# Optimization experiments

Hardware: AMD Instinct MI355X
Metric: run time of the kernel (lower is better)

Reference implementation:

```python
import jax, jax.numpy as jnp
import numpy as np

EPS = 1e-5


def _whiten(feature):
    # ZCA whitening per sample (WCT): f_w = U diag(s^-1/2) U^T (f - mean)
    b, c, h, w = feature.shape
    f = feature.reshape(b, c, h * w)
    mean = f.mean(axis=-1, keepdims=True)
    f = f - mean
    cov = jnp.einsum('bcx,bdx->bcd', f, f) / (h * w - 1)
    s, u = jnp.linalg.eigh(cov)
    s = jnp.maximum(s, EPS)
    out = jnp.einsum('bcd,bd,bed,bex->bcx', u, s ** -0.5, u, f)
    return out.reshape(b, c, h, w)


def _color(feature, target):
    # ZCA coloring: f_c = Ut diag(st^1/2) Ut^T (f - mean_f) + mean_t
    b, c, h, w = feature.shape
    f = feature.reshape(b, c, h * w)
    f = f - f.mean(axis=-1, keepdims=True)
    t = target.reshape(b, c, -1)
    tmean = t.mean(axis=-1, keepdims=True)
    tc = t - tmean
    cov = jnp.einsum('bcx,bdx->bcd', tc, tc) / (tc.shape[-1] - 1)
    s, u = jnp.linalg.eigh(cov)
    s = jnp.maximum(s, EPS)
    out = jnp.einsum('bcd,bd,bed,bex->bcx', u, s ** 0.5, u, f) + tmean
    return out.reshape(b, c, h, w)


def _patches(f, p):
    # [b,c,h,w] -> [b,c,h,w,p*p], same ordering as torch unfold(2,p).unfold(3,p)
    pad = (p - 1) // 2
    b, c, h, w = f.shape
    fp = jnp.pad(f, ((0, 0), (0, 0), (pad, pad), (pad, pad)))
    return jnp.stack([fp[:, :, i:i + h, j:j + w] for i in range(p) for j in range(p)], axis=-1)


def reference(content_feature, style_feature, style_strength, patch_size):
    p = int(patch_size)
    pad = (p - 1) // 2
    nc = _whiten(content_feature)
    ns = _whiten(style_feature)
    b, c, h, w = nc.shape
    n = h * w  # one style kernel per style spatial location (stride 1)

    # style kernels [b, n, c, p, p] and their L2 norms over (c,p,p)
    sk = _patches(ns, p).transpose(0, 2, 3, 1, 4).reshape(b, n, c, p, p)
    knorm = jnp.sqrt(jnp.sum(sk ** 2, axis=(2, 3, 4), keepdims=True))
    skn = (sk / knorm).reshape(b, n, c, p * p)

    # patch matching score == conv2d of content with normalized style kernels
    cp = _patches(nc, p)                              # [b,c,h,w,p*p]
    score = jnp.einsum('bchwk,bnck->bnhw', cp, skn)   # [b,n,h,w]

    # argmax one-hot -> gather the best-matching (un-normalized) style patch
    idx = jnp.argmax(score, axis=1)                   # [b,h,w]
    sel = jax.vmap(lambda k, i: k[i])(sk, idx.reshape(b, -1))  # [b,hw,c,p,p]
    sel = sel.reshape(b, h, w, c, p, p).transpose(0, 3, 1, 2, 4, 5)  # [b,c,h,w,p,p]

    # overlap-add == conv_transpose2d(one_hot, kernels, padding=p-1) on padded input
    buf = jnp.zeros((b, c, h + p - 1, w + p - 1), dtype=sel.dtype)
    for di in range(p):
        for dj in range(p):
            buf = buf.at[:, :, di:di + h, dj:dj + w].add(sel[:, :, :, :, di, dj])
    recon = buf[:, :, pad:pad + h, pad:pad + w]

    # overlap counts (norm_deconvolution)
    m = jnp.zeros((h + p - 1, w + p - 1), dtype=sel.dtype)
    for di in range(p):
        for dj in range(p):
            m = m.at[di:di + h, dj:dj + w].add(1.0)
    norm = m[pad:pad + h, pad:pad + w]

    reassembled = recon / norm[None, None]
    stylized = _color(reassembled, style_feature)
    return (1.0 - style_strength) * content_feature + style_strength * stylized


def setup_inputs():
    key = jax.random.key(0)
    k1, k2 = jax.random.split(key)
    B, C, H, W = 2, 256, 48, 48
    return {
        'content_feature': jax.random.normal(k1, (B, C, H, W), jnp.float32),
        'style_feature': jax.random.normal(k2, (B, C, H, W), jnp.float32),
        'style_strength': jnp.float32(1.0),
        'patch_size': 3,
    }
```

## Files before the change

kernel.cpp:

```cpp
#include <hip/hip_runtime.h>

constexpr int B_  = 2;
constexpr int C_  = 256;
constexpr int H_  = 48;
constexpr int W_  = 48;
constexpr int N_  = H_ * W_;
constexpr int PH_ = H_ + 2;
constexpr int PW_ = W_ + 2;
constexpr int NP_ = PH_ * PW_;
constexpr int CC_ = C_ * C_;
constexpr int NCH_ = 36;
constexpr int NC_  = N_ / NCH_;
constexpr int NSIT_ = 6;
constexpr int KCH_ = 9;

__device__ inline float waveRed(float v) {
  #pragma unroll
  for (int o = 32; o > 0; o >>= 1) v += __shfl_down(v, o);
  return v;
}

#define GEMM64_COMPUTE(sAT, sB, acc, ty, tx)                        \
  _Pragma("unroll")                                                 \
  for (int kk = 0; kk < 16; kk++) {                                 \
    float4 a = *(const float4*)&sAT[kk][(ty) * 4];                  \
    float4 b = *(const float4*)&sB[kk][(tx) * 4];                   \
    acc[0][0] += a.x * b.x; acc[0][1] += a.x * b.y;                 \
    acc[0][2] += a.x * b.z; acc[0][3] += a.x * b.w;                 \
    acc[1][0] += a.y * b.x; acc[1][1] += a.y * b.y;                 \
    acc[1][2] += a.y * b.z; acc[1][3] += a.y * b.w;                 \
    acc[2][0] += a.z * b.x; acc[2][1] += a.z * b.y;                 \
    acc[2][2] += a.z * b.z; acc[2][3] += a.z * b.w;                 \
    acc[3][0] += a.w * b.x; acc[3][1] += a.w * b.y;                 \
    acc[3][2] += a.w * b.z; acc[3][3] += a.w * b.w;                 \
  }


__global__ __launch_bounds__(256) void center_kernel(
    const float* __restrict__ content, const float* __restrict__ style,
    float* __restrict__ fc, float* __restrict__ fs, float* __restrict__ mean_s) {
  int t = blockIdx.x;
  int which = t / (B_ * C_);
  int bc = t % (B_ * C_);
  const float* src = which ? style : content;
  float* dst = which ? fs : fc;
  const float* row = src + (size_t)bc * N_;
  float acc = 0.f;
  for (int i = threadIdx.x; i < N_; i += 256) acc += row[i];
  __shared__ float sm[4];
  float r = waveRed(acc);
  if ((threadIdx.x & 63) == 0) sm[threadIdx.x >> 6] = r;
  __syncthreads();
  float mean = (sm[0] + sm[1] + sm[2] + sm[3]) * (1.0f / N_);
  for (int i = threadIdx.x; i < N_; i += 256) dst[(size_t)bc * N_ + i] = row[i] - mean;
  if (which == 1 && threadIdx.x == 0) mean_s[bc] = mean;
}

__global__ __launch_bounds__(256) void cov_kernel(
    const float* __restrict__ fc, const float* __restrict__ fs, float* __restrict__ pcov) {
  int z = blockIdx.z;
  int m = z & 3, ci = z >> 2;
  const float* f = (m < 2) ? (fc + (size_t)m * C_ * N_) : (fs + (size_t)(m - 2) * C_ * N_);
  int i0 = blockIdx.y * 64, j0 = blockIdx.x * 64;
  int t = threadIdx.x;
  int tx = t & 15, ty = t >> 4;
  int sr = t >> 2, skq = t & 3;
  __shared__ float sAT[16][68], sB[16][68];
  float acc[4][4] = {};
  int k0e = ci * 256 + 256;
  for (int k0 = ci * 256; k0 < k0e; k0 += 16) {
    float4 av = *(const float4*)&f[(size_t)(i0 + sr) * N_ + k0 + skq * 4];
    float4 bv = *(const float4*)&f[(size_t)(j0 + sr) * N_ + k0 + skq * 4];
    __syncthreads();
    sAT[skq * 4 + 0][sr] = av.x; sAT[skq * 4 + 1][sr] = av.y;
    sAT[skq * 4 + 2][sr] = av.z; sAT[skq * 4 + 3][sr] = av.w;
    sB[skq * 4 + 0][sr] = bv.x;  sB[skq * 4 + 1][sr] = bv.y;
    sB[skq * 4 + 2][sr] = bv.z;  sB[skq * 4 + 3][sr] = bv.w;
    __syncthreads();
    GEMM64_COMPUTE(sAT, sB, acc, ty, tx)
  }
  float* out = pcov + ((size_t)ci * 4 + m) * CC_;
  for (int u = 0; u < 4; u++)
    for (int v = 0; v < 4; v++)
      out[(size_t)(i0 + ty * 4 + u) * C_ + (j0 + tx * 4 + v)] = acc[u][v];
}

__global__ __launch_bounds__(256) void covreduce(
    const float* __restrict__ pcov, float* __restrict__ A4) {
  int t = blockIdx.x * 256 + threadIdx.x;
  float acc = 0.f;
  #pragma unroll
  for (int ci = 0; ci < KCH_; ci++) acc += pcov[(size_t)ci * 4 * CC_ + t];
  A4[t] = acc * (1.0f / (float)(N_ - 1));
}

__global__ __launch_bounds__(256) void ns_init(
    const float* __restrict__ A4, float* __restrict__ Y, float* __restrict__ Z,
    float* __restrict__ scal) {
  int m = blockIdx.y, s = blockIdx.x;
  const float* A = A4 + (size_t)m * CC_;
  float d = A[(size_t)threadIdx.x * 257];
  __shared__ float sm[4];
  float r = waveRed(d);
  if ((threadIdx.x & 63) == 0) sm[threadIdx.x >> 6] = r;
  __syncthreads();
  float trace = sm[0] + sm[1] + sm[2] + sm[3];
  float sc = 1.1f * trace / (float)C_;
  if (s == 0 && threadIdx.x == 0) scal[m] = sc;
  float inv = 1.0f / sc;
  int i0 = s * (CC_ / 16);
  for (int i = i0 + threadIdx.x; i < i0 + CC_ / 16; i += 256) {
    Y[(size_t)m * CC_ + i] = A[i] * inv;
    Z[(size_t)m * CC_ + i] = ((i >> 8) == (i & 255)) ? 1.0f : 0.0f;
  }
}

__global__ __launch_bounds__(256) void ns_stepA(
    const float* __restrict__ Z, const float* __restrict__ Y, float* __restrict__ T) {
  int m = blockIdx.z;
  const float* A = Z + (size_t)m * CC_;
  const float* Bm = Y + (size_t)m * CC_;
  float* out = T + (size_t)m * CC_;
  int i0 = blockIdx.y * 32, j0 = blockIdx.x * 32;
  int t = threadIdx.x;
  int tx = t & 15, ty = t >> 4;
  int sr = t >> 3, sc4 = t & 7;
  __shared__ float sAT[32][36], sB[32][36];
  float acc[2][2] = {};
  for (int k0 = 0; k0 < 256; k0 += 32) {
    float4 av = *(const float4*)&A[(size_t)(i0 + sr) * 256 + k0 + sc4 * 4];
    float4 bv = *(const float4*)&Bm[(size_t)(k0 + sr) * 256 + j0 + sc4 * 4];
    __syncthreads();
    sAT[sc4 * 4 + 0][sr] = av.x; sAT[sc4 * 4 + 1][sr] = av.y;
    sAT[sc4 * 4 + 2][sr] = av.z; sAT[sc4 * 4 + 3][sr] = av.w;
    *(float4*)&sB[sr][sc4 * 4] = bv;
    __syncthreads();
    #pragma unroll
    for (int kk = 0; kk < 32; kk++) {
      float2 a = *(const float2*)&sAT[kk][ty * 2];
      float2 b = *(const float2*)&sB[kk][tx * 2];
      acc[0][0] += a.x * b.x; acc[0][1] += a.x * b.y;
      acc[1][0] += a.y * b.x; acc[1][1] += a.y * b.y;
    }
    __syncthreads();
  }
  for (int u = 0; u < 2; u++)
    for (int v = 0; v < 2; v++) {
      int i = i0 + ty * 2 + u, j = j0 + tx * 2 + v;
      float d = (i == j) ? 3.0f : 0.0f;
      out[(size_t)i * 256 + j] = d - acc[u][v];
    }
}

__global__ __launch_bounds__(256) void ns_stepB(
    const float* __restrict__ Y, const float* __restrict__ Z, const float* __restrict__ T,
    float* __restrict__ Yn, float* __restrict__ Zn) {
  int z = blockIdx.z;
  int m = z & 3;
  bool doY = (z < 4);
  const float* A = (doY ? Y : T) + (size_t)m * CC_;
  const float* Bm = (doY ? T : Z) + (size_t)m * CC_;
  float* out = (doY ? Yn : Zn) + (size_t)m * CC_;
  int i0 = blockIdx.y * 32, j0 = blockIdx.x * 32;
  int t = threadIdx.x;
  int tx = t & 15, ty = t >> 4;
  int sr = t >> 3, sc4 = t & 7;
  __shared__ float sAT[32][36], sB[32][36];
  float acc[2][2] = {};
  for (int k0 = 0; k0 < 256; k0 += 32) {
    float4 av = *(const float4*)&A[(size_t)(i0 + sr) * 256 + k0 + sc4 * 4];
    float4 bv = *(const float4*)&Bm[(size_t)(k0 + sr) * 256 + j0 + sc4 * 4];
    __syncthreads();
    sAT[sc4 * 4 + 0][sr] = av.x; sAT[sc4 * 4 + 1][sr] = av.y;
    sAT[sc4 * 4 + 2][sr] = av.z; sAT[sc4 * 4 + 3][sr] = av.w;
    *(float4*)&sB[sr][sc4 * 4] = bv;
    __syncthreads();
    #pragma unroll
    for (int kk = 0; kk < 32; kk++) {
      float2 a = *(const float2*)&sAT[kk][ty * 2];
      float2 b = *(const float2*)&sB[kk][tx * 2];
      acc[0][0] += a.x * b.x; acc[0][1] += a.x * b.y;
      acc[1][0] += a.y * b.x; acc[1][1] += a.y * b.y;
    }
    __syncthreads();
  }
  for (int u = 0; u < 2; u++)
    for (int v = 0; v < 2; v++) {
      int i = i0 + ty * 2 + u, j = j0 + tx * 2 + v;
      out[(size_t)i * 256 + j] = 0.5f * acc[u][v];
    }
}

__global__ __launch_bounds__(256) void whiten_pad(
    const float* __restrict__ Zf, const float* __restrict__ scal,
    const float* __restrict__ fc, const float* __restrict__ fs,
    float* __restrict__ ncP, float* __restrict__ nsP) {
  int m = blockIdx.z;
  const float* f = (m < 2) ? (fc + (size_t)m * C_ * N_) : (fs + (size_t)(m - 2) * C_ * N_);
  int c0 = blockIdx.y * 64, x0 = blockIdx.x * 64;
  int t = threadIdx.x;
  int tx = t & 15, ty = t >> 4;
  int sr = t >> 2, skq = t & 3;
  int bkk = t & 15, bc4 = t >> 4;
  __shared__ float sAT[16][68], sB[16][68];
  float acc[4][4] = {};
  for (int k0 = 0; k0 < 256; k0 += 16) {
    float4 av = *(const float4*)&Zf[(size_t)m * CC_ + (size_t)(c0 + sr) * 256 + k0 + skq * 4];
    float4 bv = *(const float4*)&f[(size_t)(k0 + bkk) * N_ + x0 + bc4 * 4];
    __syncthreads();
    sAT[skq * 4 + 0][sr] = av.x; sAT[skq * 4 + 1][sr] = av.y;
    sAT[skq * 4 + 2][sr] = av.z; sAT[skq * 4 + 3][sr] = av.w;
    *(float4*)&sB[bkk][bc4 * 4] = bv;
    __syncthreads();
    GEMM64_COMPUTE(sAT, sB, acc, ty, tx)
  }
  float rs = rsqrtf(scal[m]);
  int b = (m < 2) ? m : (m - 2);
  for (int u = 0; u < 4; u++)
    for (int v = 0; v < 4; v++) {
      int c = c0 + ty * 4 + u, x = x0 + tx * 4 + v;
      int h = x / W_, w = x % W_;
      int pp = (h + 1) * PW_ + (w + 1);
      float val = acc[u][v] * rs;
      if (m < 2) ncP[((size_t)b * C_ + c) * NP_ + pp] = val;
      else       nsP[((size_t)b * NP_ + pp) * C_ + c] = val;
    }
}

__global__ __launch_bounds__(256) void q_kernel(const float* __restrict__ nsP, float* __restrict__ q) {
  int wid = (blockIdx.x * 256 + threadIdx.x) >> 6;
  int lane = threadIdx.x & 63;
  if (wid >= B_ * NP_) return;
  const float* v = nsP + (size_t)wid * C_;
  float acc = 0.f;
  #pragma unroll
  for (int c = lane; c < C_; c += 64) { float t = v[c]; acc += t * t; }
  acc = waveRed(acc);
  if (lane == 0) q[wid] = acc;
}

__global__ __launch_bounds__(256) void kninv_kernel(const float* __restrict__ q, float* __restrict__ kninv) {
  int t = blockIdx.x * 256 + threadIdx.x;
  if (t >= B_ * N_) return;
  int b = t / N_, n = t % N_;
  int hn = n / W_, wn = n % W_;
  const float* qb = q + (size_t)b * NP_ + hn * PW_ + wn;
  float s = 0.f;
  #pragma unroll
  for (int i = 0; i < 3; i++)
    #pragma unroll
    for (int j = 0; j < 3; j++) s += qb[i * PW_ + j];
  kninv[t] = rsqrtf(s);
}

__global__ __launch_bounds__(256) void m_kernel(
    const float* __restrict__ Asty, const float* __restrict__ Bcon, float* __restrict__ M) {
  int i0 = blockIdx.y * 128, j0 = blockIdx.x * 64;
  int t = threadIdx.x;
  int tx = t & 15, ty = t >> 4;
  int sr = t >> 1, half = t & 1;
  int bkk = t >> 4, bc4 = t & 15;
  __shared__ float sAT[16][132], sB[16][68];
  float acc[8][4] = {};
  bool arow_ok = (i0 + sr) < NP_;
  int bcol = j0 + bc4 * 4;
  bool bcol_ok4 = (bcol + 3) < NP_;
  for (int k0 = 0; k0 < 256; k0 += 16) {
    float4 a0 = {0,0,0,0}, a1 = {0,0,0,0}, bv = {0,0,0,0};
    if (arow_ok) {
      a0 = *(const float4*)&Asty[(size_t)(i0 + sr) * C_ + k0 + half * 8];
      a1 = *(const float4*)&Asty[(size_t)(i0 + sr) * C_ + k0 + half * 8 + 4];
    }
    if (bcol_ok4) bv = *(const float4*)&Bcon[(size_t)(k0 + bkk) * NP_ + bcol];
    else {
      float tmp[4] = {0,0,0,0};
      for (int j = 0; j < 4; j++) if (bcol + j < NP_) tmp[j] = Bcon[(size_t)(k0 + bkk) * NP_ + bcol + j];
      bv.x = tmp[0]; bv.y = tmp[1]; bv.z = tmp[2]; bv.w = tmp[3];
    }
    __syncthreads();
    sAT[half * 8 + 0][sr] = a0.x; sAT[half * 8 + 1][sr] = a0.y;
    sAT[half * 8 + 2][sr] = a0.z; sAT[half * 8 + 3][sr] = a0.w;
    sAT[half * 8 + 4][sr] = a1.x; sAT[half * 8 + 5][sr] = a1.y;
    sAT[half * 8 + 6][sr] = a1.z; sAT[half * 8 + 7][sr] = a1.w;
    *(float4*)&sB[bkk][bc4 * 4] = bv;
    __syncthreads();
    #pragma unroll
    for (int kk = 0; kk < 16; kk++) {
      float4 aa0 = *(const float4*)&sAT[kk][ty * 8];
      float4 aa1 = *(const float4*)&sAT[kk][ty * 8 + 4];
      float4 b = *(const float4*)&sB[kk][tx * 4];
      float ar[8] = {aa0.x, aa0.y, aa0.z, aa0.w, aa1.x, aa1.y, aa1.z, aa1.w};
      #pragma unroll
      for (int u = 0; u < 8; u++) {
        acc[u][0] += ar[u] * b.x; acc[u][1] += ar[u] * b.y;
        acc[u][2] += ar[u] * b.z; acc[u][3] += ar[u] * b.w;
      }
    }
    __syncthreads();
  }
  for (int u = 0; u < 8; u++) {
    int i = i0 + ty * 8 + u;
    if (i >= NP_) break;
    for (int v = 0; v < 4; v++) {
      int j = j0 + tx * 4 + v;
      if (j < NP_) M[(size_t)i * NP_ + j] = acc[u][v];
    }
  }
}

__global__ __launch_bounds__(256) void score_kernel(
    const float* __restrict__ M, const float* __restrict__ kninv,
    float* __restrict__ pval, int* __restrict__ pidx, int b) {
  int m = blockIdx.x * 256 + threadIdx.x;
  int h = m / W_, w = m % W_;
  int cm = h * PW_ + w;
  int n0 = blockIdx.y * NC_;
  const float* kni = kninv + (size_t)b * N_;
  float best = -3.4e38f;
  int bidx = n0;
  for (int n = n0; n < n0 + NC_; n++) {
    int hn = n / W_, wn = n % W_;
    int rn = hn * PW_ + wn;
    const float* base = M + (size_t)rn * NP_ + cm;
    float s = 0.f;
    #pragma unroll
    for (int i = 0; i < 3; i++)
      #pragma unroll
      for (int j = 0; j < 3; j++) s += base[(size_t)(i * PW_ + j) * (NP_ + 1)];
    s *= kni[n];
    if (s > best) { best = s; bidx = n; }
  }
  pval[((size_t)b * NCH_ + blockIdx.y) * N_ + m] = best;
  pidx[((size_t)b * NCH_ + blockIdx.y) * N_ + m] = bidx;
}

__global__ __launch_bounds__(256) void argmax_final(
    const float* __restrict__ pval, const int* __restrict__ pidx, int* __restrict__ idxb) {
  int t = blockIdx.x * 256 + threadIdx.x;
  if (t >= B_ * N_) return;
  int b = t / N_, m = t % N_;
  float best = -3.4e38f; int bidx = 0;
  for (int ch = 0; ch < NCH_; ch++) {
    float v = pval[((size_t)b * NCH_ + ch) * N_ + m];
    int i = pidx[((size_t)b * NCH_ + ch) * N_ + m];
    if (v > best) { best = v; bidx = i; }
  }
  idxb[t] = bidx;
}

__global__ __launch_bounds__(256) void reassemble_kernel(
    const float* __restrict__ nsP, const int* __restrict__ idxb, float* __restrict__ recon) {
  int bm = blockIdx.x;
  int b = bm / N_, m = bm % N_;
  int h = m / W_, w = m % W_;
  int c = threadIdx.x;
  float acc = 0.f; int cnt = 0;
  for (int di = 0; di < 3; di++) {
    int hs = h + 1 - di; if (hs < 0 || hs >= H_) continue;
    for (int dj = 0; dj < 3; dj++) {
      int ws = w + 1 - dj; if (ws < 0 || ws >= W_) continue;
      int n = idxb[(size_t)b * N_ + hs * W_ + ws];
      int hn = n / W_, wn = n % W_;
      int pp = (hn + di) * PW_ + (wn + dj);
      acc += nsP[((size_t)b * NP_ + pp) * C_ + c];
      cnt++;
    }
  }
  recon[((size_t)b * N_ + m) * C_ + c] = acc / (float)cnt;
}

__global__ __launch_bounds__(256) void rmean_part(const float* __restrict__ recon, float* __restrict__ pmr) {
  int b = blockIdx.y, ch = blockIdx.x, c = threadIdx.x;
  float acc = 0.f;
  int x0 = ch * (N_ / 16);
  for (int x = x0; x < x0 + (N_ / 16); x++) acc += recon[((size_t)b * N_ + x) * C_ + c];
  pmr[((size_t)b * 16 + ch) * C_ + c] = acc;
}

__global__ __launch_bounds__(256) void rmean_fin(const float* __restrict__ pmr, float* __restrict__ mr) {
  int b = blockIdx.x, c = threadIdx.x;
  float acc = 0.f;
  for (int ch = 0; ch < 16; ch++) acc += pmr[((size_t)b * 16 + ch) * C_ + c];
  mr[(size_t)b * C_ + c] = acc * (1.0f / N_);
}

__global__ __launch_bounds__(256) void color_blend(
    const float* __restrict__ Yf, const float* __restrict__ scal,
    const float* __restrict__ recon, const float* __restrict__ mr,
    const float* __restrict__ msty, const float* __restrict__ content,
    const float* __restrict__ ssp, float* __restrict__ out) {
  int b = blockIdx.z;
  int m = 2 + b;
  int c0 = blockIdx.y * 64, x0 = blockIdx.x * 64;
  int t = threadIdx.x;
  int tx = t & 15, ty = t >> 4;
  int sr = t >> 2, skq = t & 3;
  __shared__ float sAT[16][68], sB[16][68];
  float acc[4][4] = {};
  for (int k0 = 0; k0 < 256; k0 += 16) {
    float4 av = *(const float4*)&Yf[(size_t)m * CC_ + (size_t)(c0 + sr) * 256 + k0 + skq * 4];
    float4 bm4 = *(const float4*)&mr[(size_t)b * C_ + k0 + skq * 4];
    float4 bv = *(const float4*)&recon[((size_t)b * N_ + x0 + sr) * C_ + k0 + skq * 4];
    bv.x -= bm4.x; bv.y -= bm4.y; bv.z -= bm4.z; bv.w -= bm4.w;
    __syncthreads();
    sAT[skq * 4 + 0][sr] = av.x; sAT[skq * 4 + 1][sr] = av.y;
    sAT[skq * 4 + 2][sr] = av.z; sAT[skq * 4 + 3][sr] = av.w;
    sB[skq * 4 + 0][sr] = bv.x;  sB[skq * 4 + 1][sr] = bv.y;
    sB[skq * 4 + 2][sr] = bv.z;  sB[skq * 4 + 3][sr] = bv.w;
    __syncthreads();
    GEMM64_COMPUTE(sAT, sB, acc, ty, tx)
  }
  float sq = sqrtf(scal[m]);
  float ss = ssp[0];
  for (int u = 0; u < 4; u++)
    for (int v = 0; v < 4; v++) {
      int c = c0 + ty * 4 + u, x = x0 + tx * 4 + v;
      float sty = acc[u][v] * sq + msty[(size_t)b * C_ + c];
      size_t o = ((size_t)b * C_ + c) * N_ + x;
      out[o] = (1.0f - ss) * content[o] + ss * sty;
    }
}

extern "C" void kernel_launch(void* const* d_in, const int* in_sizes, int n_in,
                              void* d_out, int out_size, void* d_ws, size_t ws_size,
                              hipStream_t stream) {
  (void)in_sizes; (void)n_in; (void)out_size; (void)ws_size;
  const float* content = (const float*)d_in[0];
  const float* style   = (const float*)d_in[1];
  const float* ssp     = (const float*)d_in[2];
  float* out = (float*)d_out;
  float* W = (float*)d_ws;

  size_t off = 0;
  float* fc   = W + off; off += (size_t)B_ * C_ * N_;
  float* fs   = W + off; off += (size_t)B_ * C_ * N_;
  float* nsP  = W + off; off += (size_t)B_ * NP_ * C_;
  float* ncP  = W + off; off += (size_t)B_ * C_ * NP_;
  float* A4   = W + off; off += (size_t)4 * CC_;
  float* Ya   = W + off; off += (size_t)4 * CC_;
  float* Yb   = W + off; off += (size_t)4 * CC_;
  float* Za   = W + off; off += (size_t)4 * CC_;
  float* Zb   = W + off; off += (size_t)4 * CC_;
  float* scal = W + off; off += 4;
  float* msty = W + off; off += (size_t)B_ * C_;
  float* mr   = W + off; off += (size_t)B_ * C_;
  float* pmr  = W + off; off += (size_t)B_ * 16 * C_;
  float* q    = W + off; off += (size_t)B_ * NP_;
  float* kni  = W + off; off += (size_t)B_ * N_;
  float* pval = W + off; off += (size_t)B_ * NCH_ * N_;
  float* Mb   = W + off; off += (size_t)NP_ * NP_;
  int* pidx = (int*)(W + off); off += (size_t)B_ * NCH_ * N_;
  int* idxb = (int*)(W + off); off += (size_t)B_ * N_;
  float* pcov = Mb;
  float* T    = Mb;
  float* recon = fs;

  hipMemsetAsync(nsP, 0, (size_t)B_ * NP_ * C_ * sizeof(float), stream);
  hipMemsetAsync(ncP, 0, (size_t)B_ * C_ * NP_ * sizeof(float), stream);

  center_kernel<<<2 * B_ * C_, 256, 0, stream>>>(content, style, fc, fs, msty);
  cov_kernel<<<dim3(4, 4, 4 * KCH_), 256, 0, stream>>>(fc, fs, pcov);
  covreduce<<<4 * CC_ / 256, 256, 0, stream>>>(pcov, A4);
  ns_init<<<dim3(16, 4), 256, 0, stream>>>(A4, Ya, Za, scal);

  float *Ycur = Ya, *Zcur = Za, *Yalt = Yb, *Zalt = Zb;
  for (int it = 0; it < NSIT_; it++) {
    ns_stepA<<<dim3(8, 8, 4), 256, 0, stream>>>(Zcur, Ycur, T);
    ns_stepB<<<dim3(8, 8, 8), 256, 0, stream>>>(Ycur, Zcur, T, Yalt, Zalt);
    float* tp;
    tp = Ycur; Ycur = Yalt; Yalt = tp;
    tp = Zcur; Zcur = Zalt; Zalt = tp;
  }

  whiten_pad<<<dim3(36, 4, 4), 256, 0, stream>>>(Zcur, scal, fc, fs, ncP, nsP);
  q_kernel<<<(B_ * NP_ + 3) / 4, 256, 0, stream>>>(nsP, q);
  kninv_kernel<<<(B_ * N_ + 255) / 256, 256, 0, stream>>>(q, kni);

  for (int b = 0; b < B_; b++) {
    m_kernel<<<dim3(40, 20), 256, 0, stream>>>(
        nsP + (size_t)b * NP_ * C_, ncP + (size_t)b * C_ * NP_, Mb);
    score_kernel<<<dim3(N_ / 256, NCH_), 256, 0, stream>>>(Mb, kni, pval, pidx, b);
  }
  argmax_final<<<(B_ * N_ + 255) / 256, 256, 0, stream>>>(pval, pidx, idxb);
  reassemble_kernel<<<B_ * N_, 256, 0, stream>>>(nsP, idxb, recon);
  rmean_part<<<dim3(16, B_), 256, 0, stream>>>(recon, pmr);
  rmean_fin<<<B_, 256, 0, stream>>>(pmr, mr);
  color_blend<<<dim3(36, 4, B_), 256, 0, stream>>>(
      Ycur, scal, recon, mr, msty, content, ssp, out);
}
```

Before: 436.8 us.

## Use padded K-major layouts and 128x128 tiles in patch-match GEMM

Whiten now also writes the style features in a channel-major layout with rows padded to 2560, and content rows are padded the same way. This lets the match GEMM load both operands with aligned float4 loads and no bounds checks. The tile grows from 128x64 to 128x128 with an 8x8 register accumulator per thread, which gives more reuse per shared-memory load. The cost is an extra transposed copy with its memset, plus higher register pressure and fewer blocks per launch.

```diff
diff --git a/kernel.cpp b/kernel.cpp
--- a/kernel.cpp
+++ b/kernel.cpp
@@ -8,6 +8,7 @@
 constexpr int PH_ = H_ + 2;
 constexpr int PW_ = W_ + 2;
 constexpr int NP_ = PH_ * PW_;
+constexpr int NPS_ = 2560;
 constexpr int CC_ = C_ * C_;
 constexpr int NCH_ = 36;
 constexpr int NC_  = N_ / NCH_;
@@ -194,7 +195,7 @@
 __global__ __launch_bounds__(256) void whiten_pad(
     const float* __restrict__ Zf, const float* __restrict__ scal,
     const float* __restrict__ fc, const float* __restrict__ fs,
-    float* __restrict__ ncP, float* __restrict__ nsP) {
+    float* __restrict__ ncP, float* __restrict__ nsP, float* __restrict__ nsT) {
   int m = blockIdx.z;
   const float* f = (m < 2) ? (fc + (size_t)m * C_ * N_) : (fs + (size_t)(m - 2) * C_ * N_);
   int c0 = blockIdx.y * 64, x0 = blockIdx.x * 64;
@@ -222,8 +223,12 @@
       int h = x / W_, w = x % W_;
       int pp = (h + 1) * PW_ + (w + 1);
       float val = acc[u][v] * rs;
-      if (m < 2) ncP[((size_t)b * C_ + c) * NP_ + pp] = val;
-      else       nsP[((size_t)b * NP_ + pp) * C_ + c] = val;
+      if (m < 2) {
+        ncP[((size_t)b * C_ + c) * NPS_ + pp] = val;
+      } else {
+        nsP[((size_t)b * NP_ + pp) * C_ + c] = val;
+        nsT[((size_t)b * C_ + c) * NPS_ + pp] = val;
+      }
     }
 }
 
@@ -254,55 +259,49 @@
 }
 
 __global__ __launch_bounds__(256) void m_kernel(
-    const float* __restrict__ Asty, const float* __restrict__ Bcon, float* __restrict__ M) {
-  int i0 = blockIdx.y * 128, j0 = blockIdx.x * 64;
-  int t = threadIdx.x;
-  int tx = t & 15, ty = t >> 4;
-  int sr = t >> 1, half = t & 1;
-  int bkk = t >> 4, bc4 = t & 15;
-  __shared__ float sAT[16][132], sB[16][68];
-  float acc[8][4] = {};
-  bool arow_ok = (i0 + sr) < NP_;
-  int bcol = j0 + bc4 * 4;
-  bool bcol_ok4 = (bcol + 3) < NP_;
+    const float* __restrict__ At, const float* __restrict__ Bt, float* __restrict__ M) {
+  int i0 = blockIdx.y * 128, j0 = blockIdx.x * 128;
+  int t = threadIdx.x;
+  int tx = t & 15, ty = t >> 4;
+  __shared__ float sA[16][132], sB[16][132];
+  float acc[8][8] = {};
   for (int k0 = 0; k0 < 256; k0 += 16) {
-    float4 a0 = {0,0,0,0}, a1 = {0,0,0,0}, bv = {0,0,0,0};
-    if (arow_ok) {
-      a0 = *(const float4*)&Asty[(size_t)(i0 + sr) * C_ + k0 + half * 8];
-      a1 = *(const float4*)&Asty[(size_t)(i0 + sr) * C_ + k0 + half * 8 + 4];
-    }
-    if (bcol_ok4) bv = *(const float4*)&Bcon[(size_t)(k0 + bkk) * NP_ + bcol];
-    else {
-      float tmp[4] = {0,0,0,0};
-      for (int j = 0; j < 4; j++) if (bcol + j < NP_) tmp[j] = Bcon[(size_t)(k0 + bkk) * NP_ + bcol + j];
-      bv.x = tmp[0]; bv.y = tmp[1]; bv.z = tmp[2]; bv.w = tmp[3];
-    }
-    __syncthreads();
-    sAT[half * 8 + 0][sr] = a0.x; sAT[half * 8 + 1][sr] = a0.y;
-    sAT[half * 8 + 2][sr] = a0.z; sAT[half * 8 + 3][sr] = a0.w;
-    sAT[half * 8 + 4][sr] = a1.x; sAT[half * 8 + 5][sr] = a1.y;
-    sAT[half * 8 + 6][sr] = a1.z; sAT[half * 8 + 7][sr] = a1.w;
-    *(float4*)&sB[bkk][bc4 * 4] = bv;
+    float4 a[2], b[2];
+    #pragma unroll
+    for (int r = 0; r < 2; r++) {
+      int idx = t + r * 256;
+      int kk = idx >> 5, c4 = idx & 31;
+      a[r] = *(const float4*)&At[(size_t)(k0 + kk) * NPS_ + i0 + c4 * 4];
+      b[r] = *(const float4*)&Bt[(size_t)(k0 + kk) * NPS_ + j0 + c4 * 4];
+    }
+    __syncthreads();
+    #pragma unroll
+    for (int r = 0; r < 2; r++) {
+      int idx = t + r * 256;
+      int kk = idx >> 5, c4 = idx & 31;
+      *(float4*)&sA[kk][c4 * 4] = a[r];
+      *(float4*)&sB[kk][c4 * 4] = b[r];
+    }
     __syncthreads();
     #pragma unroll
     for (int kk = 0; kk < 16; kk++) {
-      float4 aa0 = *(const float4*)&sAT[kk][ty * 8];
-      float4 aa1 = *(const float4*)&sAT[kk][ty * 8 + 4];
-      float4 b = *(const float4*)&sB[kk][tx * 4];
-      float ar[8] = {aa0.x, aa0.y, aa0.z, aa0.w, aa1.x, aa1.y, aa1.z, aa1.w};
+      float av[8], bv[8];
+      *(float4*)&av[0] = *(const float4*)&sA[kk][ty * 8];
+      *(float4*)&av[4] = *(const float4*)&sA[kk][ty * 8 + 4];
+      *(float4*)&bv[0] = *(const float4*)&sB[kk][tx * 8];
+      *(float4*)&bv[4] = *(const float4*)&sB[kk][tx * 8 + 4];
       #pragma unroll
-      for (int u = 0; u < 8; u++) {
-        acc[u][0] += ar[u] * b.x; acc[u][1] += ar[u] * b.y;
-        acc[u][2] += ar[u] * b.z; acc[u][3] += ar[u] * b.w;
-      }
+      for (int u = 0; u < 8; u++)
+        #pragma unroll
+        for (int v = 0; v < 8; v++) acc[u][v] += av[u] * bv[v];
     }
     __syncthreads();
   }
   for (int u = 0; u < 8; u++) {
     int i = i0 + ty * 8 + u;
     if (i >= NP_) break;
-    for (int v = 0; v < 4; v++) {
-      int j = j0 + tx * 4 + v;
+    for (int v = 0; v < 8; v++) {
+      int j = j0 + tx * 8 + v;
       if (j < NP_) M[(size_t)i * NP_ + j] = acc[u][v];
     }
   }
@@ -435,7 +434,8 @@
   float* fc   = W + off; off += (size_t)B_ * C_ * N_;
   float* fs   = W + off; off += (size_t)B_ * C_ * N_;
   float* nsP  = W + off; off += (size_t)B_ * NP_ * C_;
-  float* ncP  = W + off; off += (size_t)B_ * C_ * NP_;
+  float* nsT  = W + off; off += (size_t)B_ * C_ * NPS_;
+  float* ncP  = W + off; off += (size_t)B_ * C_ * NPS_;
   float* A4   = W + off; off += (size_t)4 * CC_;
   float* Ya   = W + off; off += (size_t)4 * CC_;
   float* Yb   = W + off; off += (size_t)4 * CC_;
@@ -456,7 +456,8 @@
   float* recon = fs;
 
   hipMemsetAsync(nsP, 0, (size_t)B_ * NP_ * C_ * sizeof(float), stream);
-  hipMemsetAsync(ncP, 0, (size_t)B_ * C_ * NP_ * sizeof(float), stream);
+  hipMemsetAsync(nsT, 0, (size_t)B_ * C_ * NPS_ * sizeof(float), stream);
+  hipMemsetAsync(ncP, 0, (size_t)B_ * C_ * NPS_ * sizeof(float), stream);
 
   center_kernel<<<2 * B_ * C_, 256, 0, stream>>>(content, style, fc, fs, msty);
   cov_kernel<<<dim3(4, 4, 4 * KCH_), 256, 0, stream>>>(fc, fs, pcov);
@@ -472,13 +473,13 @@
     tp = Zcur; Zcur = Zalt; Zalt = tp;
   }
 
-  whiten_pad<<<dim3(36, 4, 4), 256, 0, stream>>>(Zcur, scal, fc, fs, ncP, nsP);
+  whiten_pad<<<dim3(36, 4, 4), 256, 0, stream>>>(Zcur, scal, fc, fs, ncP, nsP, nsT);
   q_kernel<<<(B_ * NP_ + 3) / 4, 256, 0, stream>>>(nsP, q);
   kninv_kernel<<<(B_ * N_ + 255) / 256, 256, 0, stream>>>(q, kni);
 
   for (int b = 0; b < B_; b++) {
-    m_kernel<<<dim3(40, 20), 256, 0, stream>>>(
-        nsP + (size_t)b * NP_ * C_, ncP + (size_t)b * C_ * NP_, Mb);
+    m_kernel<<<dim3(20, 20), 256, 0, stream>>>(
+        nsT + (size_t)b * C_ * NPS_, ncP + (size_t)b * C_ * NPS_, Mb);
     score_kernel<<<dim3(N_ / 256, NCH_), 256, 0, stream>>>(Mb, kni, pval, pidx, b);
   }
   argmax_final<<<(B_ * N_ + 255) / 256, 256, 0, stream>>>(pval, pidx, idxb);
```

New measurement: 462.0 us. +5.8%, slower.
